# Performance work log

Hardware: AMD Instinct MI355X
Metric: run time of the kernel (lower is better)

The kernel has to match this reference:

```python
import jax, jax.numpy as jnp
import numpy as np
import math

_EPS = 1e-5          # _SAMPLING_EPS
_K_PER_CHUNK = 32    # _TOPK_K_PER_CHUNK
_MAX_CHUNK = 32768   # _TOPK_MAX_CHUNK_SIZE
B, V = 128, 128256


def setup_inputs() -> dict:
    key = jax.random.key(0)
    ks = jax.random.split(key, 10)
    logits = jax.random.normal(ks[0], (B, V), dtype=jnp.float32) * 4.0
    temperature = jax.random.uniform(ks[1], (B,), dtype=jnp.float32) * 1.5
    top_k = jax.random.randint(ks[2], (B,), 0, 100)  # 0 => top-k disabled
    top_p = 0.5 + 0.5 * jax.random.uniform(ks[3], (B,), dtype=jnp.float32)
    output_token_counts = jax.random.randint(ks[4], (B, V), 0, 3).astype(jnp.float32)
    prompt_token_mask = jax.random.randint(ks[5], (B, V), 0, 2).astype(bool)
    presence_penalties = jax.random.uniform(ks[6], (B,), dtype=jnp.float32)
    frequency_penalties = jax.random.uniform(ks[7], (B,), dtype=jnp.float32)
    repetition_penalties = 1.0 + 0.5 * jax.random.uniform(ks[8], (B,), dtype=jnp.float32)
    u = jax.random.uniform(ks[9], (B, V), dtype=jnp.float32, minval=1e-6, maxval=1.0)
    q_samples = -jnp.log(u)  # Exponential(1) noise, vLLM random_sample convention
    return dict(logits=logits, temperature=temperature, top_k=top_k, top_p=top_p,
                output_token_counts=output_token_counts, prompt_token_mask=prompt_token_mask,
                presence_penalties=presence_penalties, frequency_penalties=frequency_penalties,
                repetition_penalties=repetition_penalties, q_samples=q_samples)


def _apply_penalties(logits, counts, prompt_mask, presence, frequency, repetition):
    counts = counts.astype(logits.dtype)
    prompt_f = prompt_mask.astype(logits.dtype)
    occurred = counts - jnp.maximum(counts - 1.0, 0.0)            # 1 if count>0 else 0
    rep_union = occurred + prompt_f
    rep_mask = rep_union - jnp.maximum(rep_union - 1.0, 0.0)      # 1 if in prompt or output
    rep = repetition[:, None]
    pos = jnp.maximum(logits, 0.0)
    neg = jnp.minimum(logits, 0.0)
    penalized = pos / rep + neg * rep
    logits = logits + rep_mask * (penalized - logits)
    logits = logits - frequency[:, None] * counts - presence[:, None] * occurred
    return logits


def _chunked_topk(logits):
    # split vocab into <=32768 chunks, top-32 per chunk (multi-core ttnn.topk emulation)
    b, v = logits.shape
    num_chunks = math.ceil(v / _MAX_CHUNK)
    chunk_size = math.ceil(v / num_chunks)
    pad = num_chunks * chunk_size - v
    x = jnp.pad(logits, ((0, 0), (0, pad)), constant_values=-np.inf) if pad else logits
    x = x.reshape(b, num_chunks, chunk_size)
    vals, inds = jax.lax.top_k(x, _K_PER_CHUNK)                   # [b, nc, k]
    inds = inds + (jnp.arange(num_chunks, dtype=inds.dtype) * chunk_size)[None, :, None]
    return vals.reshape(b, -1), inds.reshape(b, -1)               # [b, nc*k]


def _filter_topk_topp(all_values, k, p, vocab_size):
    C = all_values.shape[-1]
    probs = jax.nn.softmax(all_values, axis=-1)
    probs_sort = jnp.sort(probs, axis=-1)                         # ascending
    # top-k on candidate set
    count_k = jnp.clip(C - k.astype(jnp.int32), 0, C - 1)[:, None]
    cutoff_k = jnp.take_along_axis(probs_sort, count_k, axis=-1)
    no_k = ((k <= 0) | (k >= vocab_size))[:, None]
    cutoff_k = jnp.where(no_k, -np.inf, cutoff_k)
    all_values = jnp.where(probs < cutoff_k, -np.inf, all_values)
    # top-p on candidate set
    cumprob = jnp.cumsum(probs_sort, axis=-1)
    mask = cumprob <= (1.0 - p)[:, None]
    mask = mask.at[:, -1].set(False)
    count_p = jnp.sum(mask, axis=-1, dtype=jnp.int32)[:, None]
    cutoff_p = jnp.take_along_axis(probs_sort, count_p, axis=-1)
    all_values = jnp.where(probs < cutoff_p, -np.inf, all_values)
    return all_values


def reference(logits, temperature, top_k, top_p, output_token_counts, prompt_token_mask,
              presence_penalties, frequency_penalties, repetition_penalties, q_samples):
    logits = logits.astype(jnp.float32)
    logits = _apply_penalties(logits, output_token_counts, prompt_token_mask,
                              presence_penalties, frequency_penalties, repetition_penalties)
    greedy = jnp.argmax(logits, axis=-1)                          # [B]
    temp_eff = jnp.where(temperature < _EPS, 1.0, temperature)
    logits_t = logits / temp_eff[:, None]
    vals, inds = _chunked_topk(logits_t)                          # [B, 128] each
    filtered = _filter_topk_topp(vals, top_k, top_p, logits.shape[-1])
    probs = jax.nn.softmax(filtered, axis=-1)                     # fp32 softmax on candidates
    q_red = jnp.take_along_axis(q_samples, inds, axis=1)
    local = jnp.argmax(probs / q_red, axis=-1)                    # exponential-noise sampling
    random_sampled = jnp.take_along_axis(inds, local[:, None], axis=1)[:, 0]
    sampled = jnp.where(temperature < _EPS, greedy, random_sampled.astype(greedy.dtype))
    return sampled[:, None], probs                                # sampled_token_ids [B,1]
```

## Files before the change

kernel.cpp:

```cpp
#include <hip/hip_runtime.h>
#include <math.h>

#define BATCH   128
#define VOCAB   128256
#define NCHUNK  4
#define CSIZE   32064
#define CVEC    (CSIZE / 4)
#define T1      1024
#define NBKT    2048
#define CAP     2048
#define KSEL    32
#define CWIDTH  (NCHUNK * KSEL)
#define T2      128

__device__ __forceinline__ unsigned fenc(float f) {
    unsigned u = __float_as_uint(f);
    return (u & 0x80000000u) ? ~u : (u | 0x80000000u);
}

__device__ __forceinline__ float penalize(float l, float cnt, float pf,
                                          float rep, float freq, float pres) {
    float occ   = __fsub_rn(cnt, fmaxf(__fsub_rn(cnt, 1.0f), 0.0f));
    float ru    = __fadd_rn(occ, pf);
    float rmask = __fsub_rn(ru, fmaxf(__fsub_rn(ru, 1.0f), 0.0f));
    float pos   = fmaxf(l, 0.0f);
    float neg   = fminf(l, 0.0f);
    float pen   = __fadd_rn(__fdiv_rn(pos, rep), __fmul_rn(neg, rep));
    float p     = __fadd_rn(l, __fmul_rn(rmask, __fsub_rn(pen, l)));
    p = __fsub_rn(p, __fmul_rn(freq, cnt));
    p = __fsub_rn(p, __fmul_rn(pres, occ));
    return p;
}

__device__ __forceinline__ void load_pf(const void* pmask, long base, int i,
                                        int mtype, float pfv[4]) {
    if (mtype == 1) {
        int4 mi = ((const int4*)((const int*)pmask + base))[i];
        pfv[0] = mi.x ? 1.0f : 0.0f; pfv[1] = mi.y ? 1.0f : 0.0f;
        pfv[2] = mi.z ? 1.0f : 0.0f; pfv[3] = mi.w ? 1.0f : 0.0f;
    } else if (mtype == 2) {
        float4 mf = ((const float4*)((const float*)pmask + base))[i];
        pfv[0] = mf.x; pfv[1] = mf.y; pfv[2] = mf.z; pfv[3] = mf.w;
    } else {
        unsigned mm = ((const unsigned*)((const unsigned char*)pmask + base))[i];
        pfv[0] = (mm & 0x000000ffu) ? 1.0f : 0.0f;
        pfv[1] = (mm & 0x0000ff00u) ? 1.0f : 0.0f;
        pfv[2] = (mm & 0x00ff0000u) ? 1.0f : 0.0f;
        pfv[3] = (mm & 0xff000000u) ? 1.0f : 0.0f;
    }
}

__global__ __launch_bounds__(T1) void sampler_k1(
    const float* __restrict__ logits, const float* __restrict__ counts,
    const void* __restrict__ pmask,
    const float* __restrict__ temperature, const float* __restrict__ presence,
    const float* __restrict__ frequency, const float* __restrict__ repetition,
    float* __restrict__ g_topv, int* __restrict__ g_topi,
    float* __restrict__ g_gval, int* __restrict__ g_gidx)
{
    const int b   = blockIdx.x >> 2;
    const int c   = blockIdx.x & 3;
    const int tid = threadIdx.x;
    const long base = (long)b * VOCAB + (long)c * CSIZE;

    __shared__ unsigned hist[NBKT];
    __shared__ float    cv[CAP];
    __shared__ int      ci[CAP];
    __shared__ unsigned ccnt;
    __shared__ int      s_tb;
    __shared__ int      s_m0, s_mf;
    __shared__ float    wrv[16];
    __shared__ int      wri[16];

    for (int i = tid; i < NBKT; i += T1) hist[i] = 0;
    if (tid == 0) { ccnt = 0; s_m0 = 1; s_mf = 1; }
    __syncthreads();

    {
        const unsigned* w = (const unsigned*)pmask;
        int a01 = 1, af = 1;
        for (int i = tid; i < 4096; i += T1) {
            unsigned x = w[i];
            if (!(x == 0u || x == 1u)) a01 = 0;
            if (!(x == 0u || x == 0x3F800000u)) af = 0;
        }
        if (!a01) atomicAnd(&s_m0, 0);
        if (!af)  atomicAnd(&s_mf, 0);
    }
    __syncthreads();
    const int mtype = s_m0 ? 1 : (s_mf ? 2 : 0);

    const float temp = temperature[b];
    const float teff = (temp < 1e-5f) ? 1.0f : temp;
    const float pres = presence[b];
    const float freq = frequency[b];
    const float rep  = repetition[b];

    const float4* l4 = (const float4*)(logits + base);
    const float4* c4 = (const float4*)(counts + base);

    float gmax = -INFINITY;
    int   gidx = 0x7fffffff;

    for (int i = tid; i < CVEC; i += T1) {
        float4 lv = l4[i];
        float4 cc = c4[i];
        float pfv[4];
        load_pf(pmask, base, i, mtype, pfv);
        float le[4] = {lv.x, lv.y, lv.z, lv.w};
        float ce[4] = {cc.x, cc.y, cc.z, cc.w};
#pragma unroll
        for (int e = 0; e < 4; ++e) {
            float p = penalize(le[e], ce[e], pfv[e], rep, freq, pres);
            int idx = i * 4 + e;
            if (p > gmax) { gmax = p; gidx = idx; }
            float v = __fdiv_rn(p, teff);
            atomicAdd(&hist[fenc(v) >> 21], 1u);
        }
    }

    for (int off = 32; off > 0; off >>= 1) {
        float ov = __shfl_down(gmax, off);
        int   oi = __shfl_down(gidx, off);
        if (ov > gmax || (ov == gmax && oi < gidx)) { gmax = ov; gidx = oi; }
    }
    if ((tid & 63) == 0) { wrv[tid >> 6] = gmax; wri[tid >> 6] = gidx; }
    __syncthreads();
    if (tid == 0) {
        float bv = wrv[0]; int bi = wri[0];
        for (int w2 = 1; w2 < 16; ++w2) {
            if (wrv[w2] > bv || (wrv[w2] == bv && wri[w2] < bi)) { bv = wrv[w2]; bi = wri[w2]; }
        }
        g_gval[blockIdx.x] = bv;
        g_gidx[blockIdx.x] = c * CSIZE + bi;
    }

    if (tid < 64) {
        const int gb = tid * 32;
        unsigned gs = 0;
#pragma unroll
        for (int k = 0; k < 32; ++k) gs += hist[gb + k];
        unsigned suf = gs;
#pragma unroll
        for (int off = 1; off < 64; off <<= 1) {
            unsigned o = __shfl_down(suf, off);
            if (tid + off < 64) suf += o;
        }
        unsigned sufn = __shfl_down(suf, 1);
        if (tid == 63) sufn = 0;
        if (suf >= (unsigned)KSEL && sufn < (unsigned)KSEL) {
            unsigned acc = sufn; int tb = gb;
            for (int q = gb + 31; q >= gb; --q) {
                acc += hist[q];
                if (acc >= (unsigned)KSEL) { tb = q; break; }
            }
            s_tb = tb;
        }
    }
    __syncthreads();
    const unsigned thr = ((unsigned)s_tb) << 21;

    for (int i = tid; i < CVEC; i += T1) {
        float4 lv = l4[i];
        float4 cc = c4[i];
        float pfv[4];
        load_pf(pmask, base, i, mtype, pfv);
        float le[4] = {lv.x, lv.y, lv.z, lv.w};
        float ce[4] = {cc.x, cc.y, cc.z, cc.w};
#pragma unroll
        for (int e = 0; e < 4; ++e) {
            float p = penalize(le[e], ce[e], pfv[e], rep, freq, pres);
            float v = __fdiv_rn(p, teff);
            if (fenc(v) >= thr) {
                unsigned pos = atomicAdd(&ccnt, 1u);
                if (pos < CAP) { cv[pos] = v; ci[pos] = i * 4 + e; }
            }
        }
    }
    __syncthreads();

    unsigned m = ccnt;
    if (m > CAP) m = CAP;
    unsigned P = KSEL;
    while (P < m) P <<= 1;
    for (unsigned s = m + tid; s < P; s += T1) { cv[s] = -INFINITY; ci[s] = 0x7fffffff; }
    __syncthreads();

    for (unsigned k = 2; k <= P; k <<= 1) {
        for (unsigned j = k >> 1; j > 0; j >>= 1) {
            for (unsigned s = tid; s < P; s += T1) {
                unsigned x = s ^ j;
                if (x > s) {
                    float av = cv[s], bv = cv[x];
                    int   ai = ci[s], bi = ci[x];
                    bool xBetter = (bv > av) || (bv == av && bi < ai);
                    bool sBetter = (av > bv) || (av == bv && ai < bi);
                    bool doSwap  = ((s & k) == 0) ? xBetter : sBetter;
                    if (doSwap) { cv[s] = bv; cv[x] = av; ci[s] = bi; ci[x] = ai; }
                }
            }
            __syncthreads();
        }
    }

    if (tid < KSEL) {
        int o = blockIdx.x * KSEL + tid;
        g_topv[o] = cv[tid];
        g_topi[o] = c * CSIZE + ci[tid];
    }
}

__global__ __launch_bounds__(T2) void sampler_k2(
    const float* __restrict__ g_topv, const int* __restrict__ g_topi,
    const float* __restrict__ g_gval, const int* __restrict__ g_gidx,
    const float* __restrict__ temperature, const int* __restrict__ topk,
    const float* __restrict__ topp, const float* __restrict__ qs,
    float* __restrict__ out)
{
    const int b = blockIdx.x;
    const int j = threadIdx.x;

    __shared__ int   ix[T2];
    __shared__ float sv[T2];
    __shared__ float cum[T2];
    __shared__ float red[T2];
    __shared__ int   redi[T2];

    float val = g_topv[b * CWIDTH + j];
    int   idx = g_topi[b * CWIDTH + j];
    ix[j] = idx;

    red[j] = val; __syncthreads();
    for (int s = T2 / 2; s > 0; s >>= 1) {
        if (j < s) red[j] = fmaxf(red[j], red[j + s]);
        __syncthreads();
    }
    float m1 = red[0]; __syncthreads();
    float e = expf(__fsub_rn(val, m1));
    red[j] = e; __syncthreads();
    for (int s = T2 / 2; s > 0; s >>= 1) {
        if (j < s) red[j] = __fadd_rn(red[j], red[j + s]);
        __syncthreads();
    }
    float s1 = red[0]; __syncthreads();
    float prob = __fdiv_rn(e, s1);
    sv[j] = prob;
    __syncthreads();

    for (unsigned k = 2; k <= (unsigned)T2; k <<= 1) {
        for (unsigned jj = k >> 1; jj > 0; jj >>= 1) {
            unsigned x = (unsigned)j ^ jj;
            if (x > (unsigned)j) {
                float a = sv[j], bb = sv[x];
                bool sw = (((unsigned)j & k) == 0) ? (a > bb) : (a < bb);
                if (sw) { sv[j] = bb; sv[x] = a; }
            }
            __syncthreads();
        }
    }

    if (j == 0) {
        float a = 0.0f;
        for (int t = 0; t < T2; ++t) { a = __fadd_rn(a, sv[t]); cum[t] = a; }
    }
    __syncthreads();

    const int   k_row = topk[b];
    const float p_row = topp[b];
    int count_k = CWIDTH - k_row;
    count_k = min(max(count_k, 0), CWIDTH - 1);
    float cutoff_k = sv[count_k];
    if (k_row <= 0 || k_row >= VOCAB) cutoff_k = -INFINITY;

    float lim = __fsub_rn(1.0f, p_row);
    bool mk = (j < CWIDTH - 1) && (cum[j] <= lim);
    redi[j] = mk ? 1 : 0; __syncthreads();
    for (int s = T2 / 2; s > 0; s >>= 1) {
        if (j < s) redi[j] += redi[j + s];
        __syncthreads();
    }
    int count_p = redi[0]; __syncthreads();
    float cutoff_p = sv[count_p];

    float f = val;
    if (prob < cutoff_k) f = -INFINITY;
    if (prob < cutoff_p) f = -INFINITY;

    red[j] = f; __syncthreads();
    for (int s = T2 / 2; s > 0; s >>= 1) {
        if (j < s) red[j] = fmaxf(red[j], red[j + s]);
        __syncthreads();
    }
    float m2 = red[0]; __syncthreads();
    float e2 = (f == -INFINITY) ? 0.0f : expf(__fsub_rn(f, m2));
    red[j] = e2; __syncthreads();
    for (int s = T2 / 2; s > 0; s >>= 1) {
        if (j < s) red[j] = __fadd_rn(red[j], red[j + s]);
        __syncthreads();
    }
    float s2 = red[0]; __syncthreads();
    float pf = __fdiv_rn(e2, s2);
    out[BATCH + b * CWIDTH + j] = pf;

    float q = qs[(long)b * VOCAB + idx];
    float ratio = __fdiv_rn(pf, q);
    red[j] = ratio; redi[j] = j;
    __syncthreads();
    for (int s = T2 / 2; s > 0; s >>= 1) {
        if (j < s) {
            float o = red[j + s]; int oi = redi[j + s];
            if (o > red[j] || (o == red[j] && oi < redi[j])) { red[j] = o; redi[j] = oi; }
        }
        __syncthreads();
    }

    if (j == 0) {
        float bvv = g_gval[b * NCHUNK]; int bii = g_gidx[b * NCHUNK];
        for (int c2 = 1; c2 < NCHUNK; ++c2) {
            float w = g_gval[b * NCHUNK + c2]; int wi = g_gidx[b * NCHUNK + c2];
            if (w > bvv || (w == bvv && wi < bii)) { bvv = w; bii = wi; }
        }
        int token = ix[redi[0]];
        float tmp = temperature[b];
        int samp = (tmp < 1e-5f) ? bii : token;
        out[b] = (float)samp;
    }
}

extern "C" void kernel_launch(void* const* d_in, const int* in_sizes, int n_in,
                              void* d_out, int out_size, void* d_ws, size_t ws_size,
                              hipStream_t stream) {
    const float* logits = (const float*)d_in[0];
    const float* temp   = (const float*)d_in[1];
    const int*   topk   = (const int*)d_in[2];
    const float* topp   = (const float*)d_in[3];
    const float* counts = (const float*)d_in[4];
    const void*  pmask  = d_in[5];
    const float* pres   = (const float*)d_in[6];
    const float* freq   = (const float*)d_in[7];
    const float* rep    = (const float*)d_in[8];
    const float* qs     = (const float*)d_in[9];
    float* out = (float*)d_out;

    float* g_topv = (float*)d_ws;
    int*   g_topi = (int*)(g_topv + BATCH * CWIDTH);
    float* g_gval = (float*)(g_topi + BATCH * CWIDTH);
    int*   g_gidx = (int*)(g_gval + BATCH * NCHUNK);

    sampler_k1<<<BATCH * NCHUNK, T1, 0, stream>>>(
        logits, counts, pmask, temp, pres, freq, rep,
        g_topv, g_topi, g_gval, g_gidx);

    sampler_k2<<<BATCH, T2, 0, stream>>>(
        g_topv, g_topi, g_gval, g_gidx, temp, topk, topp, qs, out);
}
```

Before: 295.1 us.

## Keep temperature-scaled logits in registers to skip second global pass

The first pass now fully unrolls the per-thread loop (8 float4 iterations, with a tail guard for the last partial stride) and keeps the penalized, temperature-scaled values in registers. The candidate-collection pass then reads those registers instead of reloading logits, counts and the mask from global memory and recomputing the penalties. It also batches loads so more memory requests are in flight, and adds a min-blocks hint to launch bounds. The cost is 32 extra live floats per thread, which raises register pressure at 1024 threads per block.

```diff
diff --git a/kernel.cpp b/kernel.cpp
--- a/kernel.cpp
+++ b/kernel.cpp
@@ -12,6 +12,7 @@
 #define KSEL    32
 #define CWIDTH  (NCHUNK * KSEL)
 #define T2      128
+#define TAILTID 848
 
 __device__ __forceinline__ unsigned fenc(float f) {
     unsigned u = __float_as_uint(f);
@@ -32,25 +33,20 @@
     return p;
 }
 
-__device__ __forceinline__ void load_pf(const void* pmask, long base, int i,
-                                        int mtype, float pfv[4]) {
-    if (mtype == 1) {
-        int4 mi = ((const int4*)((const int*)pmask + base))[i];
-        pfv[0] = mi.x ? 1.0f : 0.0f; pfv[1] = mi.y ? 1.0f : 0.0f;
-        pfv[2] = mi.z ? 1.0f : 0.0f; pfv[3] = mi.w ? 1.0f : 0.0f;
-    } else if (mtype == 2) {
-        float4 mf = ((const float4*)((const float*)pmask + base))[i];
-        pfv[0] = mf.x; pfv[1] = mf.y; pfv[2] = mf.z; pfv[3] = mf.w;
+__device__ __forceinline__ unsigned ldmask(const void* pm, long base, int i, int mtype) {
+    if (mtype == 0) {
+        return ((const unsigned*)((const unsigned char*)pm + base))[i];
+    } else if (mtype == 1) {
+        int4 m = ((const int4*)((const int*)pm + base))[i];
+        return (m.x ? 1u : 0u) | (m.y ? 0x100u : 0u) | (m.z ? 0x10000u : 0u) | (m.w ? 0x1000000u : 0u);
     } else {
-        unsigned mm = ((const unsigned*)((const unsigned char*)pmask + base))[i];
-        pfv[0] = (mm & 0x000000ffu) ? 1.0f : 0.0f;
-        pfv[1] = (mm & 0x0000ff00u) ? 1.0f : 0.0f;
-        pfv[2] = (mm & 0x00ff0000u) ? 1.0f : 0.0f;
-        pfv[3] = (mm & 0xff000000u) ? 1.0f : 0.0f;
-    }
-}
-
-__global__ __launch_bounds__(T1) void sampler_k1(
+        float4 f = ((const float4*)((const float*)pm + base))[i];
+        return ((f.x != 0.f) ? 1u : 0u) | ((f.y != 0.f) ? 0x100u : 0u) |
+               ((f.z != 0.f) ? 0x10000u : 0u) | ((f.w != 0.f) ? 0x1000000u : 0u);
+    }
+}
+
+__global__ __launch_bounds__(T1, 4) void sampler_k1(
     const float* __restrict__ logits, const float* __restrict__ counts,
     const void* __restrict__ pmask,
     const float* __restrict__ temperature, const float* __restrict__ presence,
@@ -102,22 +98,67 @@
     float gmax = -INFINITY;
     int   gidx = 0x7fffffff;
 
-    for (int i = tid; i < CVEC; i += T1) {
-        float4 lv = l4[i];
-        float4 cc = c4[i];
-        float pfv[4];
-        load_pf(pmask, base, i, mtype, pfv);
-        float le[4] = {lv.x, lv.y, lv.z, lv.w};
-        float ce[4] = {cc.x, cc.y, cc.z, cc.w};
-#pragma unroll
-        for (int e = 0; e < 4; ++e) {
-            float p = penalize(le[e], ce[e], pfv[e], rep, freq, pres);
-            int idx = i * 4 + e;
-            if (p > gmax) { gmax = p; gidx = idx; }
-            float v = __fdiv_rn(p, teff);
-            atomicAdd(&hist[fenc(v) >> 21], 1u);
-        }
-    }
+    const bool tail = tid < TAILTID;
+
+    float4 v0, v1, v2, v3, v4, v5, v6, v7;
+    v7.x = v7.y = v7.z = v7.w = 0.0f;
+
+#define PROC1(Lv, Cv, Mv, Vv, I0) do {                                          \
+        float p_;                                                               \
+        p_ = penalize((Lv).x, (Cv).x, ((Mv) & 0x000000ffu) ? 1.0f : 0.0f,       \
+                      rep, freq, pres);                                         \
+        if (p_ > gmax) { gmax = p_; gidx = (I0) * 4 + 0; }                      \
+        (Vv).x = __fdiv_rn(p_, teff);                                           \
+        atomicAdd(&hist[fenc((Vv).x) >> 21], 1u);                               \
+        p_ = penalize((Lv).y, (Cv).y, ((Mv) & 0x0000ff00u) ? 1.0f : 0.0f,       \
+                      rep, freq, pres);                                         \
+        if (p_ > gmax) { gmax = p_; gidx = (I0) * 4 + 1; }                      \
+        (Vv).y = __fdiv_rn(p_, teff);                                           \
+        atomicAdd(&hist[fenc((Vv).y) >> 21], 1u);                               \
+        p_ = penalize((Lv).z, (Cv).z, ((Mv) & 0x00ff0000u) ? 1.0f : 0.0f,       \
+                      rep, freq, pres);                                         \
+        if (p_ > gmax) { gmax = p_; gidx = (I0) * 4 + 2; }                      \
+        (Vv).z = __fdiv_rn(p_, teff);                                           \
+        atomicAdd(&hist[fenc((Vv).z) >> 21], 1u);                               \
+        p_ = penalize((Lv).w, (Cv).w, ((Mv) & 0xff000000u) ? 1.0f : 0.0f,       \
+                      rep, freq, pres);                                         \
+        if (p_ > gmax) { gmax = p_; gidx = (I0) * 4 + 3; }                      \
+        (Vv).w = __fdiv_rn(p_, teff);                                           \
+        atomicAdd(&hist[fenc((Vv).w) >> 21], 1u);                               \
+    } while (0)
+
+    {
+        float4 L0 = l4[tid],          L1 = l4[tid + T1];
+        float4 L2 = l4[tid + 2 * T1], L3 = l4[tid + 3 * T1];
+        float4 C0 = c4[tid],          C1 = c4[tid + T1];
+        float4 C2 = c4[tid + 2 * T1], C3 = c4[tid + 3 * T1];
+        unsigned M0 = ldmask(pmask, base, tid,          mtype);
+        unsigned M1 = ldmask(pmask, base, tid + T1,     mtype);
+        unsigned M2 = ldmask(pmask, base, tid + 2 * T1, mtype);
+        unsigned M3 = ldmask(pmask, base, tid + 3 * T1, mtype);
+        PROC1(L0, C0, M0, v0, tid);
+        PROC1(L1, C1, M1, v1, tid + T1);
+        PROC1(L2, C2, M2, v2, tid + 2 * T1);
+        PROC1(L3, C3, M3, v3, tid + 3 * T1);
+    }
+    {
+        float4 L4 = l4[tid + 4 * T1], L5 = l4[tid + 5 * T1], L6 = l4[tid + 6 * T1];
+        float4 C4 = c4[tid + 4 * T1], C5 = c4[tid + 5 * T1], C6 = c4[tid + 6 * T1];
+        unsigned M4 = ldmask(pmask, base, tid + 4 * T1, mtype);
+        unsigned M5 = ldmask(pmask, base, tid + 5 * T1, mtype);
+        unsigned M6 = ldmask(pmask, base, tid + 6 * T1, mtype);
+        float4 L7, C7; unsigned M7 = 0;
+        if (tail) {
+            L7 = l4[tid + 7 * T1];
+            C7 = c4[tid + 7 * T1];
+            M7 = ldmask(pmask, base, tid + 7 * T1, mtype);
+        }
+        PROC1(L4, C4, M4, v4, tid + 4 * T1);
+        PROC1(L5, C5, M5, v5, tid + 5 * T1);
+        PROC1(L6, C6, M6, v6, tid + 6 * T1);
+        if (tail) PROC1(L7, C7, M7, v7, tid + 7 * T1);
+    }
+#undef PROC1
 
     for (int off = 32; off > 0; off >>= 1) {
         float ov = __shfl_down(gmax, off);
@@ -160,23 +201,34 @@
     __syncthreads();
     const unsigned thr = ((unsigned)s_tb) << 21;
 
-    for (int i = tid; i < CVEC; i += T1) {
-        float4 lv = l4[i];
-        float4 cc = c4[i];
-        float pfv[4];
-        load_pf(pmask, base, i, mtype, pfv);
-        float le[4] = {lv.x, lv.y, lv.z, lv.w};
-        float ce[4] = {cc.x, cc.y, cc.z, cc.w};
-#pragma unroll
-        for (int e = 0; e < 4; ++e) {
-            float p = penalize(le[e], ce[e], pfv[e], rep, freq, pres);
-            float v = __fdiv_rn(p, teff);
-            if (fenc(v) >= thr) {
-                unsigned pos = atomicAdd(&ccnt, 1u);
-                if (pos < CAP) { cv[pos] = v; ci[pos] = i * 4 + e; }
-            }
-        }
-    }
+#define COLL(Vv, I0) do {                                                       \
+        if (fenc((Vv).x) >= thr) {                                              \
+            unsigned pos_ = atomicAdd(&ccnt, 1u);                               \
+            if (pos_ < CAP) { cv[pos_] = (Vv).x; ci[pos_] = (I0) * 4 + 0; }     \
+        }                                                                       \
+        if (fenc((Vv).y) >= thr) {                                              \
+            unsigned pos_ = atomicAdd(&ccnt, 1u);                               \
+            if (pos_ < CAP) { cv[pos_] = (Vv).y; ci[pos_] = (I0) * 4 + 1; }     \
+        }                                                                       \
+        if (fenc((Vv).z) >= thr) {                                              \
+            unsigned pos_ = atomicAdd(&ccnt, 1u);                               \
+            if (pos_ < CAP) { cv[pos_] = (Vv).z; ci[pos_] = (I0) * 4 + 2; }     \
+        }                                                                       \
+        if (fenc((Vv).w) >= thr) {                                              \
+            unsigned pos_ = atomicAdd(&ccnt, 1u);                               \
+            if (pos_ < CAP) { cv[pos_] = (Vv).w; ci[pos_] = (I0) * 4 + 3; }     \
+        }                                                                       \
+    } while (0)
+
+    COLL(v0, tid);
+    COLL(v1, tid + T1);
+    COLL(v2, tid + 2 * T1);
+    COLL(v3, tid + 3 * T1);
+    COLL(v4, tid + 4 * T1);
+    COLL(v5, tid + 5 * T1);
+    COLL(v6, tid + 6 * T1);
+    if (tail) COLL(v7, tid + 7 * T1);
+#undef COLL
     __syncthreads();
 
     unsigned m = ccnt;
```

After: 274.7 us. 1.07x faster.

## Skip non-candidate vectors in second pass via per-vector max bucket codes

Applied to the files above, without the earlier changes.

The first pass now stores, in shared memory, the highest histogram bucket of each 4-element vector, and the second pass only reloads and re-penalizes vectors whose code reaches the threshold bucket. This avoids re-reading the whole logits/counts/mask chunk from global memory a second time. Histogramming now uses the penalized logit before temperature division, so the per-element division is deferred to selected candidates only. The mask-type branching is hoisted out of the loop through templated specializations. Bucketing on pre-temperature values assumes positive temperature preserves ordering, and the extra 16 KB of shared memory may lower occupancy.

```diff
diff --git a/kernel.cpp b/kernel.cpp
--- a/kernel.cpp
+++ b/kernel.cpp
@@ -32,22 +32,129 @@
     return p;
 }
 
-__device__ __forceinline__ void load_pf(const void* pmask, long base, int i,
-                                        int mtype, float pfv[4]) {
-    if (mtype == 1) {
-        int4 mi = ((const int4*)((const int*)pmask + base))[i];
-        pfv[0] = mi.x ? 1.0f : 0.0f; pfv[1] = mi.y ? 1.0f : 0.0f;
-        pfv[2] = mi.z ? 1.0f : 0.0f; pfv[3] = mi.w ? 1.0f : 0.0f;
-    } else if (mtype == 2) {
-        float4 mf = ((const float4*)((const float*)pmask + base))[i];
-        pfv[0] = mf.x; pfv[1] = mf.y; pfv[2] = mf.z; pfv[3] = mf.w;
-    } else {
-        unsigned mm = ((const unsigned*)((const unsigned char*)pmask + base))[i];
-        pfv[0] = (mm & 0x000000ffu) ? 1.0f : 0.0f;
-        pfv[1] = (mm & 0x0000ff00u) ? 1.0f : 0.0f;
-        pfv[2] = (mm & 0x00ff0000u) ? 1.0f : 0.0f;
-        pfv[3] = (mm & 0xff000000u) ? 1.0f : 0.0f;
-    }
+template<int MT> struct MaskT;
+template<> struct MaskT<0> { using T = unsigned; };
+template<> struct MaskT<1> { using T = int4; };
+template<> struct MaskT<2> { using T = float4; };
+
+__device__ __forceinline__ unsigned mpack(unsigned m) { return m; }
+__device__ __forceinline__ unsigned mpack(int4 m) {
+    return (m.x ? 1u : 0u) | (m.y ? 0x100u : 0u) |
+           (m.z ? 0x10000u : 0u) | (m.w ? 0x1000000u : 0u);
+}
+__device__ __forceinline__ unsigned mpack(float4 m) {
+    return ((m.x != 0.f) ? 1u : 0u) | ((m.y != 0.f) ? 0x100u : 0u) |
+           ((m.z != 0.f) ? 0x10000u : 0u) | ((m.w != 0.f) ? 0x1000000u : 0u);
+}
+
+template<int MT>
+__device__ __forceinline__ const typename MaskT<MT>::T* mbase(const void* pm, long base) {
+    if constexpr (MT == 0)
+        return (const typename MaskT<0>::T*)((const unsigned char*)pm + base);
+    else if constexpr (MT == 1)
+        return (const typename MaskT<1>::T*)((const int*)pm + base);
+    else
+        return (const typename MaskT<2>::T*)((const float*)pm + base);
+}
+
+template<int MT>
+__device__ __forceinline__ void chunk_scan(
+    const float4* __restrict__ l4, const float4* __restrict__ c4,
+    const void* __restrict__ pmask, long base, int tid, int bid, int c,
+    float teff, float pres, float freq, float rep,
+    unsigned* hist, unsigned short* gcode,
+    float* cv, int* ci, unsigned* ccnt, int* s_tb,
+    float* wrv, int* wri,
+    float* __restrict__ g_gval, int* __restrict__ g_gidx)
+{
+    using MR = typename MaskT<MT>::T;
+    const MR* mp = mbase<MT>(pmask, base);
+
+    float gmax = -INFINITY;
+    int   gidx = 0x7fffffff;
+
+    for (int i = tid; i < CVEC; i += T1) {
+        float4 lv = l4[i];
+        float4 cc = c4[i];
+        unsigned mm = mpack(mp[i]);
+        float le[4] = {lv.x, lv.y, lv.z, lv.w};
+        float ce[4] = {cc.x, cc.y, cc.z, cc.w};
+        unsigned gc = 0;
+#pragma unroll
+        for (int e = 0; e < 4; ++e) {
+            float pf = ((mm >> (8 * e)) & 0xffu) ? 1.0f : 0.0f;
+            float p  = penalize(le[e], ce[e], pf, rep, freq, pres);
+            int idx  = i * 4 + e;
+            if (p > gmax) { gmax = p; gidx = idx; }
+            unsigned bk = fenc(p) >> 21;
+            if (bk > gc) gc = bk;
+            atomicAdd(&hist[bk], 1u);
+        }
+        gcode[i] = (unsigned short)gc;
+    }
+
+    for (int off = 32; off > 0; off >>= 1) {
+        float ov = __shfl_down(gmax, off);
+        int   oi = __shfl_down(gidx, off);
+        if (ov > gmax || (ov == gmax && oi < gidx)) { gmax = ov; gidx = oi; }
+    }
+    if ((tid & 63) == 0) { wrv[tid >> 6] = gmax; wri[tid >> 6] = gidx; }
+    __syncthreads();
+    if (tid == 0) {
+        float bv = wrv[0]; int bi = wri[0];
+        for (int w2 = 1; w2 < 16; ++w2) {
+            if (wrv[w2] > bv || (wrv[w2] == bv && wri[w2] < bi)) { bv = wrv[w2]; bi = wri[w2]; }
+        }
+        g_gval[bid] = bv;
+        g_gidx[bid] = c * CSIZE + bi;
+    }
+
+    if (tid < 64) {
+        const int gb = tid * 32;
+        unsigned gs = 0;
+#pragma unroll
+        for (int k = 0; k < 32; ++k) gs += hist[gb + k];
+        unsigned suf = gs;
+#pragma unroll
+        for (int off = 1; off < 64; off <<= 1) {
+            unsigned o = __shfl_down(suf, off);
+            if (tid + off < 64) suf += o;
+        }
+        unsigned sufn = __shfl_down(suf, 1);
+        if (tid == 63) sufn = 0;
+        if (suf >= (unsigned)KSEL && sufn < (unsigned)KSEL) {
+            unsigned acc = sufn; int tb = gb;
+            for (int q = gb + 31; q >= gb; --q) {
+                acc += hist[q];
+                if (acc >= (unsigned)KSEL) { tb = q; break; }
+            }
+            *s_tb = tb;
+        }
+    }
+    __syncthreads();
+    const unsigned tbv = (unsigned)(*s_tb);
+    const unsigned thr = tbv << 21;
+
+    for (int k = 0; k < 8; ++k) {
+        int g = tid + k * T1;
+        if (g < CVEC && (unsigned)gcode[g] >= tbv) {
+            float4 L = l4[g];
+            float4 C = c4[g];
+            unsigned mm = mpack(mp[g]);
+            float le[4] = {L.x, L.y, L.z, L.w};
+            float ce[4] = {C.x, C.y, C.z, C.w};
+#pragma unroll
+            for (int e = 0; e < 4; ++e) {
+                float pf = ((mm >> (8 * e)) & 0xffu) ? 1.0f : 0.0f;
+                float p  = penalize(le[e], ce[e], pf, rep, freq, pres);
+                if (fenc(p) >= thr) {
+                    unsigned pos = atomicAdd(ccnt, 1u);
+                    if (pos < CAP) { cv[pos] = __fdiv_rn(p, teff); ci[pos] = g * 4 + e; }
+                }
+            }
+        }
+    }
+    __syncthreads();
 }
 
 __global__ __launch_bounds__(T1) void sampler_k1(
@@ -64,6 +171,7 @@
     const long base = (long)b * VOCAB + (long)c * CSIZE;
 
     __shared__ unsigned hist[NBKT];
+    __shared__ unsigned short gcode[CVEC];
     __shared__ float    cv[CAP];
     __shared__ int      ci[CAP];
     __shared__ unsigned ccnt;
@@ -99,85 +207,15 @@
     const float4* l4 = (const float4*)(logits + base);
     const float4* c4 = (const float4*)(counts + base);
 
-    float gmax = -INFINITY;
-    int   gidx = 0x7fffffff;
-
-    for (int i = tid; i < CVEC; i += T1) {
-        float4 lv = l4[i];
-        float4 cc = c4[i];
-        float pfv[4];
-        load_pf(pmask, base, i, mtype, pfv);
-        float le[4] = {lv.x, lv.y, lv.z, lv.w};
-        float ce[4] = {cc.x, cc.y, cc.z, cc.w};
-#pragma unroll
-        for (int e = 0; e < 4; ++e) {
-            float p = penalize(le[e], ce[e], pfv[e], rep, freq, pres);
-            int idx = i * 4 + e;
-            if (p > gmax) { gmax = p; gidx = idx; }
-            float v = __fdiv_rn(p, teff);
-            atomicAdd(&hist[fenc(v) >> 21], 1u);
-        }
-    }
-
-    for (int off = 32; off > 0; off >>= 1) {
-        float ov = __shfl_down(gmax, off);
-        int   oi = __shfl_down(gidx, off);
-        if (ov > gmax || (ov == gmax && oi < gidx)) { gmax = ov; gidx = oi; }
-    }
-    if ((tid & 63) == 0) { wrv[tid >> 6] = gmax; wri[tid >> 6] = gidx; }
-    __syncthreads();
-    if (tid == 0) {
-        float bv = wrv[0]; int bi = wri[0];
-        for (int w2 = 1; w2 < 16; ++w2) {
-            if (wrv[w2] > bv || (wrv[w2] == bv && wri[w2] < bi)) { bv = wrv[w2]; bi = wri[w2]; }
-        }
-        g_gval[blockIdx.x] = bv;
-        g_gidx[blockIdx.x] = c * CSIZE + bi;
-    }
-
-    if (tid < 64) {
-        const int gb = tid * 32;
-        unsigned gs = 0;
-#pragma unroll
-        for (int k = 0; k < 32; ++k) gs += hist[gb + k];
-        unsigned suf = gs;
-#pragma unroll
-        for (int off = 1; off < 64; off <<= 1) {
-            unsigned o = __shfl_down(suf, off);
-            if (tid + off < 64) suf += o;
-        }
-        unsigned sufn = __shfl_down(suf, 1);
-        if (tid == 63) sufn = 0;
-        if (suf >= (unsigned)KSEL && sufn < (unsigned)KSEL) {
-            unsigned acc = sufn; int tb = gb;
-            for (int q = gb + 31; q >= gb; --q) {
-                acc += hist[q];
-                if (acc >= (unsigned)KSEL) { tb = q; break; }
-            }
-            s_tb = tb;
-        }
-    }
-    __syncthreads();
-    const unsigned thr = ((unsigned)s_tb) << 21;
-
-    for (int i = tid; i < CVEC; i += T1) {
-        float4 lv = l4[i];
-        float4 cc = c4[i];
-        float pfv[4];
-        load_pf(pmask, base, i, mtype, pfv);
-        float le[4] = {lv.x, lv.y, lv.z, lv.w};
-        float ce[4] = {cc.x, cc.y, cc.z, cc.w};
-#pragma unroll
-        for (int e = 0; e < 4; ++e) {
-            float p = penalize(le[e], ce[e], pfv[e], rep, freq, pres);
-            float v = __fdiv_rn(p, teff);
-            if (fenc(v) >= thr) {
-                unsigned pos = atomicAdd(&ccnt, 1u);
-                if (pos < CAP) { cv[pos] = v; ci[pos] = i * 4 + e; }
-            }
-        }
-    }
-    __syncthreads();
+    if (mtype == 1)
+        chunk_scan<1>(l4, c4, pmask, base, tid, blockIdx.x, c, teff, pres, freq, rep,
+                      hist, gcode, cv, ci, &ccnt, &s_tb, wrv, wri, g_gval, g_gidx);
+    else if (mtype == 0)
+        chunk_scan<0>(l4, c4, pmask, base, tid, blockIdx.x, c, teff, pres, freq, rep,
+                      hist, gcode, cv, ci, &ccnt, &s_tb, wrv, wri, g_gval, g_gidx);
+    else
+        chunk_scan<2>(l4, c4, pmask, base, tid, blockIdx.x, c, teff, pres, freq, rep,
+                      hist, gcode, cv, ci, &ccnt, &s_tb, wrv, wri, g_gval, g_gidx);
 
     unsigned m = ccnt;
     if (m > CAP) m = CAP;
```

Result: faster. 277.2 us (-6.1%).
